# Optimization experiments

Hardware: AMD Instinct MI355X
Metric: run time of the kernel (lower is better)

Reference implementation:

```python
import jax, jax.numpy as jnp
import numpy as np

B, T, UD, YD, ZD, HD, L = 1024, 1024, 16, 16, 16, 128, 2


def setup_inputs() -> dict:
    key = jax.random.key(0)
    ks = iter(jax.random.split(key, 40))
    r = lambda *s: jax.random.normal(next(ks), s, jnp.float32) * 0.05
    inp = dict(
        u=jax.random.normal(next(ks), (B, UD, T), jnp.float32),
        y=jax.random.normal(next(ks), (B, YD, T), jnp.float32),
        h0=jax.random.uniform(next(ks), (L, B, HD), jnp.float32),
        phi_u_w0=r(HD, UD), phi_u_b0=r(HD), phi_u_w1=r(HD, HD), phi_u_b1=r(HD),
        dynn_w0=r(HD, 2 * HD), dynn_b0=r(HD), dynn_w1=r(HD, HD), dynn_b1=r(HD),
        x_mean_w=r(ZD, HD), x_mean_b=r(ZD),
        x_logvar_w=r(ZD, HD), x_logvar_b=r(ZD),
        phi_x_w0=r(HD, 2 * ZD), phi_x_b0=r(HD), phi_x_w1=r(HD, HD), phi_x_b1=r(HD),
        menn_w0=r(HD, HD), menn_b0=r(HD), menn_w1=r(YD, HD), menn_b1=r(YD),
        gru_wih=r(L, 3 * HD, HD), gru_whh=r(L, 3 * HD, HD),
        C=r(YD, ZD),
    )
    return inp


def _mlp2(x, w0, b0, w1, b1):
    # Linear -> ReLU -> Linear (torch Linear: y = x W^T + b)
    return jax.nn.relu(x @ w0.T + b0) @ w1.T + b1


def reference(u, y, h0,
              phi_u_w0, phi_u_b0, phi_u_w1, phi_u_b1,
              dynn_w0, dynn_b0, dynn_w1, dynn_b1,
              x_mean_w, x_mean_b, x_logvar_w, x_logvar_b,
              phi_x_w0, phi_x_b0, phi_x_w1, phi_x_b1,
              menn_w0, menn_b0, menn_w1, menn_b1,
              gru_wih, gru_whh, C):
    uT = jnp.moveaxis(u, 2, 0)  # (T, B, UD)
    yT = jnp.moveaxis(y, 2, 0)  # (T, B, YD)

    def step(h, xy):
        u_t, y_t = xy
        phi_u_t = _mlp2(u_t, phi_u_w0, phi_u_b0, phi_u_w1, phi_u_b1)  # (B, HD)
        dphi = _mlp2(jnp.concatenate([phi_u_t, h[-1]], axis=1),
                     dynn_w0, dynn_b0, dynn_w1, dynn_b1)
        x_mean = dphi @ x_mean_w.T + x_mean_b      # (B, ZD)
        x_logvar = dphi @ x_logvar_w.T + x_logvar_b
        # single-step multi-layer GRU (no bias), PyTorch gate order r,z,n
        x = phi_u_t
        hs = []
        for l in range(L):
            gi = x @ gru_wih[l].T          # (B, 3HD)
            gh = h[l] @ gru_whh[l].T
            ir, iz, inn = jnp.split(gi, 3, axis=1)
            hr, hz, hn = jnp.split(gh, 3, axis=1)
            rg = jax.nn.sigmoid(ir + hr)
            zg = jax.nn.sigmoid(iz + hz)
            ng = jnp.tanh(inn + rg * hn)
            hl = (1.0 - zg) * ng + zg * h[l]
            hs.append(hl)
            x = hl
        h_new = jnp.stack(hs, axis=0)
        # mpnt_wt >= 10 branch: NN measurement + physics measurement C @ x_mean
        phi_x = _mlp2(jnp.concatenate([x_mean, x_logvar], axis=1),
                      phi_x_w0, phi_x_b0, phi_x_w1, phi_x_b1)
        y_hat = _mlp2(phi_x, menn_w0, menn_b0, menn_w1, menn_b1) + x_mean @ C.T
        loss_t = jnp.sum((y_hat - y_t) ** 2)
        return h_new, loss_t

    _, losses = jax.lax.scan(step, h0, (uT, yT))
    return jnp.sum(losses)
```

## Files before the change

### kernel.cpp

```cpp
#include <hip/hip_runtime.h>
#include <hip/hip_bf16.h>

typedef unsigned short u16;
typedef unsigned int u32;
using short8 = __attribute__((ext_vector_type(8))) short;
using f32x4  = __attribute__((ext_vector_type(4))) float;

#define DEVINL static __device__ __forceinline__

DEVINL float bf2f(u16 u){
  union { unsigned int i; float f; } x; x.i = ((unsigned int)u) << 16; return x.f;
}
DEVINL u16 f2bf(float f){
  union { float f; unsigned int i; } x; x.f = f;
  unsigned int i = x.i;
  return (u16)((i + 0x7FFFu + ((i >> 16) & 1u)) >> 16);
}
DEVINL u16 f2bf1(float f){
  __hip_bfloat16 b = __float2bfloat16(f);
  u16 u; __builtin_memcpy(&u, &b, 2); return u;
}
DEVINL float fast_sigm(float x){
  float e = __builtin_amdgcn_exp2f(x * -1.442695041f);
  return __builtin_amdgcn_rcpf(1.f + e);
}
DEVINL float fast_tanh(float x){
  x = fminf(fmaxf(x, -10.f), 10.f);
  float e = __builtin_amdgcn_exp2f(x * -2.885390082f);
  return (1.f - e) * __builtin_amdgcn_rcpf(1.f + e);
}
DEVINL f32x4 zero4(){ f32x4 z = {0.f, 0.f, 0.f, 0.f}; return z; }

DEVINL f32x4 mfma16(short8 a, short8 b, f32x4 c){
  return __builtin_amdgcn_mfma_f32_16x16x32_bf16(a, b, c, 0, 0, 0);
}

DEVINL short8 frag_ld(const u16* base, int stride){
  int l = threadIdx.x & 63;
  return *(const short8*)(base + (l & 15) * stride + ((l >> 4) << 3));
}
DEVINL short8 gfrag(const u16* rowbase, int stride, int ks){
  int l = threadIdx.x & 63;
  return *(const short8*)(rowbase + (size_t)(l & 15) * stride + ks * 32 + ((l >> 4) << 3));
}

DEVINL void acc_store_lds(u16* dst, int stride, int col_base, f32x4 acc, float bias, bool relu){
  int l = threadIdx.x & 63;
  int col = col_base + (l & 15);
  int row0 = (l >> 4) * 4;
  #pragma unroll
  for (int r = 0; r < 4; r++){
    float v = acc[r] + bias;
    if (relu) v = fmaxf(v, 0.f);
    dst[(row0 + r) * stride + col] = f2bf(v);
  }
}

DEVINL void stage_weights(u16* dst, const float* src, int N, int K, int Kp){
  int stride = Kp + 8;
  if (Kp > K){
    int padw = Kp - K;
    for (int i = threadIdx.x; i < N * padw; i += blockDim.x){
      int n = i / padw, k = K + (i - (i / padw) * padw);
      dst[n * stride + k] = 0;
    }
  }
  for (int i = threadIdx.x * 4; i < N * K; i += blockDim.x * 4){
    float4 v = *(const float4*)(src + i);
    int n = i / K, k = i - n * K;
    u16* d = dst + n * stride + k;
    d[0] = f2bf(v.x); d[1] = f2bf(v.y); d[2] = f2bf(v.z); d[3] = f2bf(v.w);
  }
}

__global__ __launch_bounds__(256) void k_inith(const float* __restrict__ h0, u16* __restrict__ hst){
  int i = blockIdx.x * 256 + threadIdx.x;
  if (i < 2 * 1024 * 128) hst[i] = f2bf(h0[i]);
}

__global__ __launch_bounds__(512, 4) void k_phiu(const float* __restrict__ u,
    const float* __restrict__ w0, const float* __restrict__ b0,
    const float* __restrict__ w1, const float* __restrict__ b1,
    u16* __restrict__ phi, int t0, int Tc){
  __shared__ __align__(16) u16 w0s[128 * 40];
  __shared__ __align__(16) u16 w1s[128 * 136];
  __shared__ __align__(16) u16 buf[8][16 * 136];
  stage_weights(w0s, w0, 128, 16, 32);
  stage_weights(w1s, w1, 128, 128, 128);
  int wv = threadIdx.x >> 6, l = threadIdx.x & 63;
  u16* mybuf = buf[wv];
  float b0v[8], b1v[8];
  #pragma unroll
  for (int nt = 0; nt < 8; nt++){
    b0v[nt] = b0[nt * 16 + (l & 15)];
    b1v[nt] = b1[nt * 16 + (l & 15)];
  }
  __syncthreads();
  int tpb = Tc >> 4;
  int ntile = 1024 * tpb;
  int stride = gridDim.x * 8;
  for (int tile = blockIdx.x * 8 + wv; tile < ntile; tile += stride){
    int b = tile / tpb;
    int tt = (tile - b * tpb) << 4;
    int t = l & 15, kb = l >> 4;
    #pragma unroll
    for (int j = 0; j < 4; j++){
      int k = kb + j * 4;
      mybuf[t * 136 + k] = f2bf(u[(size_t)(b * 16 + k) * 1024 + t0 + tt + t]);
      mybuf[t * 136 + 16 + k] = 0;
    }
    short8 a0 = frag_ld(mybuf, 136);
    f32x4 acc[8];
    #pragma unroll
    for (int nt = 0; nt < 8; nt++)
      acc[nt] = mfma16(a0, frag_ld(w0s + nt * 16 * 40, 40), zero4());
    #pragma unroll
    for (int nt = 0; nt < 8; nt++)
      acc_store_lds(mybuf, 136, nt * 16, acc[nt], b0v[nt], true);
    f32x4 a2[8];
    #pragma unroll
    for (int nt = 0; nt < 8; nt++) a2[nt] = zero4();
    #pragma unroll
    for (int ks = 0; ks < 4; ks++){
      short8 a = frag_ld(mybuf + ks * 32, 136);
      #pragma unroll
      for (int nt = 0; nt < 8; nt++)
        a2[nt] = mfma16(a, frag_ld(w1s + nt * 16 * 136 + ks * 32, 136), a2[nt]);
    }
    #pragma unroll
    for (int nt = 0; nt < 8; nt++)
      acc_store_lds(mybuf, 136, nt * 16, a2[nt], b1v[nt], false);
    u16* dst = phi + (size_t)(b * Tc + tt) * 128;
    #pragma unroll
    for (int j = 0; j < 4; j++){
      int c = j * 64 + l;
      int row = c >> 4, k = (c & 15) * 8;
      *(short8*)(dst + row * 128 + k) = *(const short8*)(mybuf + row * 136 + k);
    }
  }
}

__global__ __launch_bounds__(256, 1) void k_gru(const u16* __restrict__ phi,
    const float* __restrict__ gwih, const float* __restrict__ gwhh,
    u16* __restrict__ hst, u16* __restrict__ Hs, int Tc){
  __shared__ __align__(16) u16 wi0[384 * 136];
  __shared__ __align__(16) u16 h0s[2][16 * 136];
  __shared__ __align__(16) u16 h1s[2][16 * 136];
  __shared__ __align__(16) u16 pb[4][16 * 136];
  const int l = threadIdx.x & 63;
  const int wv = threadIdx.x >> 6;
  const int b0 = blockIdx.x * 16;
  const int m0 = (l >> 4) * 4;
  const int cc = l & 15;
  const int nb = wv * 32;

  stage_weights(wi0, gwih, 384, 128, 128);

  const float* srcs[3] = { gwhh, gwih + 49152, gwhh + 49152 };
  short8 Wr[3][3][2][4];
  #pragma unroll
  for (int mm = 0; mm < 3; mm++){
    #pragma unroll
    for (int g = 0; g < 3; g++){
      #pragma unroll
      for (int nt = 0; nt < 2; nt++){
        int n = g * 128 + nb + nt * 16 + cc;
        #pragma unroll
        for (int ks = 0; ks < 4; ks++){
          const float* p = srcs[mm] + (size_t)n * 128 + ks * 32 + ((l >> 4) << 3);
          float4 va = *(const float4*)p;
          float4 vb = *(const float4*)(p + 4);
          short8 f;
          f[0] = (short)f2bf(va.x); f[1] = (short)f2bf(va.y);
          f[2] = (short)f2bf(va.z); f[3] = (short)f2bf(va.w);
          f[4] = (short)f2bf(vb.x); f[5] = (short)f2bf(vb.y);
          f[6] = (short)f2bf(vb.z); f[7] = (short)f2bf(vb.w);
          Wr[mm][g][nt][ks] = f;
        }
      }
    }
  }
  const int row = threadIdx.x >> 4, k0 = (threadIdx.x & 15) * 8;
  *(uint4*)(&h0s[0][row * 136 + k0]) = *(const uint4*)(hst + (size_t)(b0 + row) * 128 + k0);
  *(uint4*)(&h1s[0][row * 136 + k0]) = *(const uint4*)(hst + 131072 + (size_t)(b0 + row) * 128 + k0);
  float hp0[2][4], hp1[2][4];
  #pragma unroll
  for (int nt = 0; nt < 2; nt++)
    #pragma unroll
    for (int r = 0; r < 4; r++){
      hp0[nt][r] = bf2f(hst[(size_t)(b0 + m0 + r) * 128 + nb + nt * 16 + cc]);
      hp1[nt][r] = bf2f(hst[131072 + (size_t)(b0 + m0 + r) * 128 + nb + nt * 16 + cc]);
    }
  const u16* pL = phi + (size_t)(b0 + row) * Tc * 128 + k0;
  u16* Hp = Hs + (size_t)(b0 + row) * Tc * 128 + k0;
  *(uint4*)(&pb[0][row * 136 + k0]) = *(const uint4*)(pL);
  *(uint4*)(&pb[1][row * 136 + k0]) = *(const uint4*)(pL + 128);
  uint4 pfA = *(const uint4*)(pL + 2 * 128);
  uint4 pfB = *(const uint4*)(pL + 3 * 128);
  __syncthreads();

  auto ITER = [&](int i, int P, int q, uint4& pf){
    short8 a0[4];
    #pragma unroll
    for (int ks = 0; ks < 4; ks++) a0[ks] = frag_ld(h0s[P] + ks * 32, 136);
    if (i > 0){
      short8 a1[4];
      #pragma unroll
      for (int ks = 0; ks < 4; ks++) a1[ks] = frag_ld(h1s[P ^ 1] + ks * 32, 136);
      *(uint4*)(Hp + (size_t)(i - 1) * 128) = *(const uint4*)(&h1s[P ^ 1][row * 136 + k0]);
      f32x4 cr[2], cz[2], cin[2], chn[2];
      #pragma unroll
      for (int nt = 0; nt < 2; nt++){ cr[nt]=zero4(); cz[nt]=zero4(); cin[nt]=zero4(); chn[nt]=zero4(); }
      #pragma unroll
      for (int ks = 0; ks < 4; ks++)
        #pragma unroll
        for (int nt = 0; nt < 2; nt++){
          cr[nt]  = mfma16(a0[ks], Wr[1][0][nt][ks], cr[nt]);
          cr[nt]  = mfma16(a1[ks], Wr[2][0][nt][ks], cr[nt]);
          cz[nt]  = mfma16(a0[ks], Wr[1][1][nt][ks], cz[nt]);
          cz[nt]  = mfma16(a1[ks], Wr[2][1][nt][ks], cz[nt]);
          cin[nt] = mfma16(a0[ks], Wr[1][2][nt][ks], cin[nt]);
          chn[nt] = mfma16(a1[ks], Wr[2][2][nt][ks], chn[nt]);
        }
      #pragma unroll
      for (int nt = 0; nt < 2; nt++)
        #pragma unroll
        for (int r = 0; r < 4; r++){
          float rg = fast_sigm(cr[nt][r]);
          float zg = fast_sigm(cz[nt][r]);
          float ng = fast_tanh(cin[nt][r] + rg * chn[nt][r]);
          float hv = zg * (hp1[nt][r] - ng) + ng;
          hp1[nt][r] = hv;
          h1s[P][(m0 + r) * 136 + nb + nt * 16 + cc] = f2bf1(hv);
        }
    }
    if (i < Tc){
      short8 ap[4];
      #pragma unroll
      for (int ks = 0; ks < 4; ks++) ap[ks] = frag_ld(pb[q] + ks * 32, 136);
      f32x4 cr[2], cz[2], cin[2], chn[2];
      #pragma unroll
      for (int nt = 0; nt < 2; nt++){ cr[nt]=zero4(); cz[nt]=zero4(); cin[nt]=zero4(); chn[nt]=zero4(); }
      #pragma unroll
      for (int ks = 0; ks < 4; ks++)
        #pragma unroll
        for (int nt = 0; nt < 2; nt++){
          cr[nt]  = mfma16(ap[ks], frag_ld(wi0 + (0 * 128 + nb + nt * 16) * 136 + ks * 32, 136), cr[nt]);
          cr[nt]  = mfma16(a0[ks], Wr[0][0][nt][ks], cr[nt]);
          cz[nt]  = mfma16(ap[ks], frag_ld(wi0 + (1 * 128 + nb + nt * 16) * 136 + ks * 32, 136), cz[nt]);
          cz[nt]  = mfma16(a0[ks], Wr[0][1][nt][ks], cz[nt]);
          cin[nt] = mfma16(ap[ks], frag_ld(wi0 + (2 * 128 + nb + nt * 16) * 136 + ks * 32, 136), cin[nt]);
          chn[nt] = mfma16(a0[ks], Wr[0][2][nt][ks], chn[nt]);
        }
      if (i + 2 < Tc) *(uint4*)(&pb[(q + 2) & 3][row * 136 + k0]) = pf;
      if (i + 4 < Tc) pf = *(const uint4*)(pL + (size_t)(i + 4) * 128);
      #pragma unroll
      for (int nt = 0; nt < 2; nt++)
        #pragma unroll
        for (int r = 0; r < 4; r++){
          float rg = fast_sigm(cr[nt][r]);
          float zg = fast_sigm(cz[nt][r]);
          float ng = fast_tanh(cin[nt][r] + rg * chn[nt][r]);
          float hv = zg * (hp0[nt][r] - ng) + ng;
          hp0[nt][r] = hv;
          h0s[P ^ 1][(m0 + r) * 136 + nb + nt * 16 + cc] = f2bf1(hv);
        }
    }
    asm volatile("s_waitcnt lgkmcnt(0)" ::: "memory");
    __builtin_amdgcn_s_barrier();
    asm volatile("" ::: "memory");
  };

  for (int i = 0; i < Tc; i += 4){
    ITER(i + 0, 0, 0, pfA);
    ITER(i + 1, 1, 1, pfB);
    ITER(i + 2, 0, 2, pfA);
    ITER(i + 3, 1, 3, pfB);
  }
  ITER(Tc, 0, 0, pfA);
  *(uint4*)(hst + (size_t)(b0 + row) * 128 + k0) = *(const uint4*)(&h0s[0][row * 136 + k0]);
  *(uint4*)(hst + 131072 + (size_t)(b0 + row) * 128 + k0) = *(const uint4*)(&h1s[0][row * 136 + k0]);
}

__global__ __launch_bounds__(512, 2) void k_c1(const u16* __restrict__ phi, const u16* __restrict__ Hs,
    const float* __restrict__ dw0, const float* __restrict__ db0,
    const float* __restrict__ dw1, const float* __restrict__ db1,
    const float* __restrict__ xmw, const float* __restrict__ xmb,
    const float* __restrict__ xlw, const float* __restrict__ xlb,
    u16* __restrict__ xmlv, int Tc){
  __shared__ __align__(16) u16 w0s[128 * 264];
  __shared__ __align__(16) u16 w1s[128 * 136];
  __shared__ __align__(16) u16 xws[32 * 136];
  __shared__ __align__(16) u16 buf[8][16 * 136];
  stage_weights(w0s, dw0, 128, 256, 256);
  stage_weights(w1s, dw1, 128, 128, 128);
  stage_weights(xws, xmw, 16, 128, 128);
  stage_weights(xws + 16 * 136, xlw, 16, 128, 128);
  int wv = threadIdx.x >> 6, l = threadIdx.x & 63;
  u16* mybuf = buf[wv];
  float b0v[8], b1v[8];
  #pragma unroll
  for (int nt = 0; nt < 8; nt++){
    b0v[nt] = db0[nt * 16 + (l & 15)];
    b1v[nt] = db1[nt * 16 + (l & 15)];
  }
  float bxm = xmb[l & 15], bxl = xlb[l & 15];
  __syncthreads();
  int tpb = Tc >> 4;
  int ntile = 1024 * tpb;
  int stride = gridDim.x * 8;
  for (int tile = blockIdx.x * 8 + wv; tile < ntile; tile += stride){
    int b = tile / tpb;
    int tt = (tile - b * tpb) << 4;
    size_t rbase = (size_t)(b * Tc + tt);
    const u16* ap = phi + rbase * 128;
    const u16* hp = Hs + rbase * 128;
    f32x4 acc[8];
    #pragma unroll
    for (int nt = 0; nt < 8; nt++) acc[nt] = zero4();
    #pragma unroll
    for (int ks = 0; ks < 8; ks++){
      short8 a = (ks < 4) ? gfrag(ap, 128, ks) : gfrag(hp, 128, ks - 4);
      #pragma unroll
      for (int nt = 0; nt < 8; nt++)
        acc[nt] = mfma16(a, frag_ld(w0s + nt * 16 * 264 + ks * 32, 264), acc[nt]);
    }
    #pragma unroll
    for (int nt = 0; nt < 8; nt++)
      acc_store_lds(mybuf, 136, nt * 16, acc[nt], b0v[nt], true);
    f32x4 a2[8];
    #pragma unroll
    for (int nt = 0; nt < 8; nt++) a2[nt] = zero4();
    #pragma unroll
    for (int ks = 0; ks < 4; ks++){
      short8 a = frag_ld(mybuf + ks * 32, 136);
      #pragma unroll
      for (int nt = 0; nt < 8; nt++)
        a2[nt] = mfma16(a, frag_ld(w1s + nt * 16 * 136 + ks * 32, 136), a2[nt]);
    }
    #pragma unroll
    for (int nt = 0; nt < 8; nt++)
      acc_store_lds(mybuf, 136, nt * 16, a2[nt], b1v[nt], false);
    f32x4 am = zero4(), al = zero4();
    #pragma unroll
    for (int ks = 0; ks < 4; ks++){
      short8 a = frag_ld(mybuf + ks * 32, 136);
      am = mfma16(a, frag_ld(xws + ks * 32, 136), am);
      al = mfma16(a, frag_ld(xws + 16 * 136 + ks * 32, 136), al);
    }
    acc_store_lds(mybuf, 136, 0, am, bxm, false);
    acc_store_lds(mybuf, 136, 16, al, bxl, false);
    u16* dst = xmlv + rbase * 32;
    int c = l;
    int row = c >> 2, k = (c & 3) * 8;
    *(short8*)(dst + row * 32 + k) = *(const short8*)(mybuf + row * 136 + k);
  }
}

__global__ __launch_bounds__(512, 2) void k_c2(const u16* __restrict__ xmlv, const float* __restrict__ y,
    const float* __restrict__ pw0, const float* __restrict__ pb0,
    const float* __restrict__ pw1, const float* __restrict__ pb1,
    const float* __restrict__ mw0, const float* __restrict__ mb0,
    const float* __restrict__ mw1, const float* __restrict__ mb1,
    const float* __restrict__ Cw, float* __restrict__ out, int t0, int Tc){
  __shared__ __align__(16) u16 pw0s[128 * 40];
  __shared__ __align__(16) u16 pw1s[128 * 136];
  __shared__ __align__(16) u16 mw0s[128 * 136];
  __shared__ __align__(16) u16 mw1s[16 * 136];
  __shared__ __align__(16) u16 Cs[16 * 40];
  __shared__ __align__(16) u16 buf[8][16 * 136];
  stage_weights(pw0s, pw0, 128, 32, 32);
  stage_weights(pw1s, pw1, 128, 128, 128);
  stage_weights(mw0s, mw0, 128, 128, 128);
  stage_weights(mw1s, mw1, 16, 128, 128);
  stage_weights(Cs, Cw, 16, 16, 32);
  int wv = threadIdx.x >> 6, l = threadIdx.x & 63;
  u16* mybuf = buf[wv];
  float bp0v[8], bp1v[8], bm0v[8];
  #pragma unroll
  for (int nt = 0; nt < 8; nt++){
    bp0v[nt] = pb0[nt * 16 + (l & 15)];
    bp1v[nt] = pb1[nt * 16 + (l & 15)];
    bm0v[nt] = mb0[nt * 16 + (l & 15)];
  }
  float bm1 = mb1[l & 15];
  __syncthreads();
  float lacc = 0.f;
  int tpb = Tc >> 4;
  int ntile = 1024 * tpb;
  int stride = gridDim.x * 8;
  for (int tile = blockIdx.x * 8 + wv; tile < ntile; tile += stride){
    int b = tile / tpb;
    int tt = (tile - b * tpb) << 4;
    size_t rbase = (size_t)(b * Tc + tt);
    const u16* xp = xmlv + rbase * 32;
    short8 a0 = gfrag(xp, 32, 0);
    f32x4 acc[8];
    #pragma unroll
    for (int nt = 0; nt < 8; nt++)
      acc[nt] = mfma16(a0, frag_ld(pw0s + nt * 16 * 40, 40), zero4());
    #pragma unroll
    for (int nt = 0; nt < 8; nt++)
      acc_store_lds(mybuf, 136, nt * 16, acc[nt], bp0v[nt], true);
    f32x4 a2[8];
    #pragma unroll
    for (int nt = 0; nt < 8; nt++) a2[nt] = zero4();
    #pragma unroll
    for (int ks = 0; ks < 4; ks++){
      short8 a = frag_ld(mybuf + ks * 32, 136);
      #pragma unroll
      for (int nt = 0; nt < 8; nt++)
        a2[nt] = mfma16(a, frag_ld(pw1s + nt * 16 * 136 + ks * 32, 136), a2[nt]);
    }
    #pragma unroll
    for (int nt = 0; nt < 8; nt++)
      acc_store_lds(mybuf, 136, nt * 16, a2[nt], bp1v[nt], false);
    f32x4 a3[8];
    #pragma unroll
    for (int nt = 0; nt < 8; nt++) a3[nt] = zero4();
    #pragma unroll
    for (int ks = 0; ks < 4; ks++){
      short8 a = frag_ld(mybuf + ks * 32, 136);
      #pragma unroll
      for (int nt = 0; nt < 8; nt++)
        a3[nt] = mfma16(a, frag_ld(mw0s + nt * 16 * 136 + ks * 32, 136), a3[nt]);
    }
    #pragma unroll
    for (int nt = 0; nt < 8; nt++)
      acc_store_lds(mybuf, 136, nt * 16, a3[nt], bm0v[nt], true);
    f32x4 ay = zero4();
    #pragma unroll
    for (int ks = 0; ks < 4; ks++){
      short8 a = frag_ld(mybuf + ks * 32, 136);
      ay = mfma16(a, frag_ld(mw1s + ks * 32, 136), ay);
    }
    f32x4 ac = mfma16(a0, frag_ld(Cs, 40), zero4());
    #pragma unroll
    for (int r = 0; r < 4; r++){
      float yh = ay[r] + bm1 + ac[r];
      int m = (l >> 4) * 4 + r, j = l & 15;
      float d = yh - y[(size_t)(b * 16 + j) * 1024 + t0 + tt + m];
      lacc += d * d;
    }
  }
  #pragma unroll
  for (int off = 32; off > 0; off >>= 1)
    lacc += __shfl_down(lacc, off);
  if (l == 0) atomicAdd(out, lacc);
}

extern "C" void kernel_launch(void* const* d_in, const int* in_sizes, int n_in,
                              void* d_out, int out_size, void* d_ws, size_t ws_size,
                              hipStream_t stream){
  const float* u    = (const float*)d_in[0];
  const float* y    = (const float*)d_in[1];
  const float* h0   = (const float*)d_in[2];
  const float* puw0 = (const float*)d_in[3];
  const float* pub0 = (const float*)d_in[4];
  const float* puw1 = (const float*)d_in[5];
  const float* pub1 = (const float*)d_in[6];
  const float* dw0  = (const float*)d_in[7];
  const float* db0  = (const float*)d_in[8];
  const float* dw1  = (const float*)d_in[9];
  const float* db1  = (const float*)d_in[10];
  const float* xmw  = (const float*)d_in[11];
  const float* xmb  = (const float*)d_in[12];
  const float* xlw  = (const float*)d_in[13];
  const float* xlb  = (const float*)d_in[14];
  const float* pxw0 = (const float*)d_in[15];
  const float* pxb0 = (const float*)d_in[16];
  const float* pxw1 = (const float*)d_in[17];
  const float* pxb1 = (const float*)d_in[18];
  const float* mw0  = (const float*)d_in[19];
  const float* mb0  = (const float*)d_in[20];
  const float* mw1  = (const float*)d_in[21];
  const float* mb1  = (const float*)d_in[22];
  const float* gwih = (const float*)d_in[23];
  const float* gwhh = (const float*)d_in[24];
  const float* Cw   = (const float*)d_in[25];

  char* w = (char*)d_ws;
  u16* hst = (u16*)w; w += (size_t)2 * 1024 * 128 * 2;
  size_t head = (size_t)2 * 1024 * 128 * 2 + 4096;
  size_t avail = (ws_size > head) ? (ws_size - head) : 0;
  int Tc = 1024;
  while (Tc > 64 && (size_t)1024 * (size_t)Tc * (128 + 128 + 32) * 2 > avail) Tc >>= 1;
  u16* phi  = (u16*)w; w += (size_t)1024 * Tc * 128 * 2;
  u16* Hs   = (u16*)w; w += (size_t)1024 * Tc * 128 * 2;
  u16* xmlv = (u16*)w; w += (size_t)1024 * Tc * 32 * 2;

  hipMemsetAsync(d_out, 0, sizeof(float), stream);
  k_inith<<<1024, 256, 0, stream>>>(h0, hst);
  for (int t0 = 0; t0 < 1024; t0 += Tc){
    k_phiu<<<512, 512, 0, stream>>>(u, puw0, pub0, puw1, pub1, phi, t0, Tc);
    k_gru<<<64, 256, 0, stream>>>(phi, gwih, gwhh, hst, Hs, Tc);
    k_c1<<<256, 512, 0, stream>>>(phi, Hs, dw0, db0, dw1, db1, xmw, xmb, xlw, xlb, xmlv, Tc);
    k_c2<<<256, 512, 0, stream>>>(xmlv, y, pxw0, pxb0, pxw1, pxb1, mw0, mb0, mw1, mb1, Cw,
                                  (float*)d_out, t0, Tc);
  }
}
```

Before: 3.378 ms.

## Split GRU layers across two warp groups with register-resident weights

The GRU kernel now launches 512 threads per block instead of 256. The first four waves compute layer 0 and the other four compute layer 1 of the wavefront-pipelined recurrence. Each group holds its own input and hidden weights in registers, so the LDS-staged layer-0 input weights and their per-step LDS fragment loads are gone. s_setprio is raised around the MFMA chains. This should roughly halve the serial MFMA work per wave on the recurrent critical path, at the cost of more waves competing for the same CU and the barrier now spanning eight waves.

```diff
diff --git a/kernel.cpp b/kernel.cpp
--- a/kernel.cpp
+++ b/kernel.cpp
@@ -140,26 +140,24 @@
   }
 }
 
-__global__ __launch_bounds__(256, 1) void k_gru(const u16* __restrict__ phi,
+__global__ __launch_bounds__(512, 1) void k_gru(const u16* __restrict__ phi,
     const float* __restrict__ gwih, const float* __restrict__ gwhh,
     u16* __restrict__ hst, u16* __restrict__ Hs, int Tc){
-  __shared__ __align__(16) u16 wi0[384 * 136];
   __shared__ __align__(16) u16 h0s[2][16 * 136];
   __shared__ __align__(16) u16 h1s[2][16 * 136];
   __shared__ __align__(16) u16 pb[4][16 * 136];
   const int l = threadIdx.x & 63;
-  const int wv = threadIdx.x >> 6;
+  const bool isL0 = (threadIdx.x < 256);
+  const int wv4 = (threadIdx.x >> 6) & 3;
   const int b0 = blockIdx.x * 16;
   const int m0 = (l >> 4) * 4;
   const int cc = l & 15;
-  const int nb = wv * 32;
-
-  stage_weights(wi0, gwih, 384, 128, 128);
-
-  const float* srcs[3] = { gwhh, gwih + 49152, gwhh + 49152 };
-  short8 Wr[3][3][2][4];
-  #pragma unroll
-  for (int mm = 0; mm < 3; mm++){
+  const int nb = wv4 * 32;
+
+  const float* wsrc[2] = { isL0 ? gwih : gwih + 49152, isL0 ? gwhh : gwhh + 49152 };
+  short8 Wr[2][3][2][4];
+  #pragma unroll
+  for (int mm = 0; mm < 2; mm++){
     #pragma unroll
     for (int g = 0; g < 3; g++){
       #pragma unroll
@@ -167,7 +165,7 @@
         int n = g * 128 + nb + nt * 16 + cc;
         #pragma unroll
         for (int ks = 0; ks < 4; ks++){
-          const float* p = srcs[mm] + (size_t)n * 128 + ks * 32 + ((l >> 4) << 3);
+          const float* p = wsrc[mm] + (size_t)n * 128 + ks * 32 + ((l >> 4) << 3);
           float4 va = *(const float4*)p;
           float4 vb = *(const float4*)(p + 4);
           short8 f;
@@ -180,91 +178,108 @@
       }
     }
   }
-  const int row = threadIdx.x >> 4, k0 = (threadIdx.x & 15) * 8;
-  *(uint4*)(&h0s[0][row * 136 + k0]) = *(const uint4*)(hst + (size_t)(b0 + row) * 128 + k0);
-  *(uint4*)(&h1s[0][row * 136 + k0]) = *(const uint4*)(hst + 131072 + (size_t)(b0 + row) * 128 + k0);
-  float hp0[2][4], hp1[2][4];
+  {
+    int row = threadIdx.x >> 5, k0 = (threadIdx.x & 31) * 4;
+    *(uint2*)(&h0s[0][row * 136 + k0]) = *(const uint2*)(hst + (size_t)(b0 + row) * 128 + k0);
+    *(uint2*)(&h1s[0][row * 136 + k0]) = *(const uint2*)(hst + 131072 + (size_t)(b0 + row) * 128 + k0);
+  }
+  const u16* hbase = hst + (isL0 ? 0 : 131072);
+  float hp[2][4];
   #pragma unroll
   for (int nt = 0; nt < 2; nt++)
     #pragma unroll
-    for (int r = 0; r < 4; r++){
-      hp0[nt][r] = bf2f(hst[(size_t)(b0 + m0 + r) * 128 + nb + nt * 16 + cc]);
-      hp1[nt][r] = bf2f(hst[131072 + (size_t)(b0 + m0 + r) * 128 + nb + nt * 16 + cc]);
-    }
-  const u16* pL = phi + (size_t)(b0 + row) * Tc * 128 + k0;
-  u16* Hp = Hs + (size_t)(b0 + row) * Tc * 128 + k0;
-  *(uint4*)(&pb[0][row * 136 + k0]) = *(const uint4*)(pL);
-  *(uint4*)(&pb[1][row * 136 + k0]) = *(const uint4*)(pL + 128);
-  uint4 pfA = *(const uint4*)(pL + 2 * 128);
-  uint4 pfB = *(const uint4*)(pL + 3 * 128);
+    for (int r = 0; r < 4; r++)
+      hp[nt][r] = bf2f(hbase[(size_t)(b0 + m0 + r) * 128 + nb + nt * 16 + cc]);
+
+  const int gp = threadIdx.x & 255;
+  const int srow = gp >> 4, sk = (gp & 15) * 8;
+  const u16* pL0 = phi + (size_t)(b0 + srow) * Tc * 128 + sk;
+  u16* Hp = Hs + (size_t)(b0 + srow) * Tc * 128 + sk;
+  uint4 pfA, pfB;
+  if (isL0){
+    *(uint4*)(&pb[0][srow * 136 + sk]) = *(const uint4*)(pL0);
+    *(uint4*)(&pb[1][srow * 136 + sk]) = *(const uint4*)(pL0 + 128);
+    pfA = *(const uint4*)(pL0 + 2 * 128);
+    pfB = *(const uint4*)(pL0 + 3 * 128);
+  }
   __syncthreads();
 
   auto ITER = [&](int i, int P, int q, uint4& pf){
-    short8 a0[4];
-    #pragma unroll
-    for (int ks = 0; ks < 4; ks++) a0[ks] = frag_ld(h0s[P] + ks * 32, 136);
-    if (i > 0){
-      short8 a1[4];
-      #pragma unroll
-      for (int ks = 0; ks < 4; ks++) a1[ks] = frag_ld(h1s[P ^ 1] + ks * 32, 136);
-      *(uint4*)(Hp + (size_t)(i - 1) * 128) = *(const uint4*)(&h1s[P ^ 1][row * 136 + k0]);
-      f32x4 cr[2], cz[2], cin[2], chn[2];
-      #pragma unroll
-      for (int nt = 0; nt < 2; nt++){ cr[nt]=zero4(); cz[nt]=zero4(); cin[nt]=zero4(); chn[nt]=zero4(); }
-      #pragma unroll
-      for (int ks = 0; ks < 4; ks++)
-        #pragma unroll
-        for (int nt = 0; nt < 2; nt++){
-          cr[nt]  = mfma16(a0[ks], Wr[1][0][nt][ks], cr[nt]);
-          cr[nt]  = mfma16(a1[ks], Wr[2][0][nt][ks], cr[nt]);
-          cz[nt]  = mfma16(a0[ks], Wr[1][1][nt][ks], cz[nt]);
-          cz[nt]  = mfma16(a1[ks], Wr[2][1][nt][ks], cz[nt]);
-          cin[nt] = mfma16(a0[ks], Wr[1][2][nt][ks], cin[nt]);
-          chn[nt] = mfma16(a1[ks], Wr[2][2][nt][ks], chn[nt]);
+    if (isL0){
+      if (i < Tc){
+        short8 a0[4], ap[4];
+        #pragma unroll
+        for (int ks = 0; ks < 4; ks++){
+          a0[ks] = frag_ld(h0s[P] + ks * 32, 136);
+          ap[ks] = frag_ld(pb[q] + ks * 32, 136);
         }
-      #pragma unroll
-      for (int nt = 0; nt < 2; nt++)
-        #pragma unroll
-        for (int r = 0; r < 4; r++){
-          float rg = fast_sigm(cr[nt][r]);
-          float zg = fast_sigm(cz[nt][r]);
-          float ng = fast_tanh(cin[nt][r] + rg * chn[nt][r]);
-          float hv = zg * (hp1[nt][r] - ng) + ng;
-          hp1[nt][r] = hv;
-          h1s[P][(m0 + r) * 136 + nb + nt * 16 + cc] = f2bf1(hv);
+        f32x4 cr[2], cz[2], cin[2], chn[2];
+        #pragma unroll
+        for (int nt = 0; nt < 2; nt++){ cr[nt]=zero4(); cz[nt]=zero4(); cin[nt]=zero4(); chn[nt]=zero4(); }
+        __builtin_amdgcn_s_setprio(1);
+        #pragma unroll
+        for (int ks = 0; ks < 4; ks++)
+          #pragma unroll
+          for (int nt = 0; nt < 2; nt++){
+            cr[nt]  = mfma16(ap[ks], Wr[0][0][nt][ks], cr[nt]);
+            cr[nt]  = mfma16(a0[ks], Wr[1][0][nt][ks], cr[nt]);
+            cz[nt]  = mfma16(ap[ks], Wr[0][1][nt][ks], cz[nt]);
+            cz[nt]  = mfma16(a0[ks], Wr[1][1][nt][ks], cz[nt]);
+            cin[nt] = mfma16(ap[ks], Wr[0][2][nt][ks], cin[nt]);
+            chn[nt] = mfma16(a0[ks], Wr[1][2][nt][ks], chn[nt]);
+          }
+        __builtin_amdgcn_s_setprio(0);
+        if (i + 2 < Tc) *(uint4*)(&pb[(q + 2) & 3][srow * 136 + sk]) = pf;
+        if (i + 4 < Tc) pf = *(const uint4*)(pL0 + (size_t)(i + 4) * 128);
+        #pragma unroll
+        for (int nt = 0; nt < 2; nt++)
+          #pragma unroll
+          for (int r = 0; r < 4; r++){
+            float rg = fast_sigm(cr[nt][r]);
+            float zg = fast_sigm(cz[nt][r]);
+            float ng = fast_tanh(cin[nt][r] + rg * chn[nt][r]);
+            float hv = zg * (hp[nt][r] - ng) + ng;
+            hp[nt][r] = hv;
+            h0s[P ^ 1][(m0 + r) * 136 + nb + nt * 16 + cc] = f2bf1(hv);
+          }
+      }
+    } else {
+      if (i > 0){
+        short8 a0[4], a1[4];
+        #pragma unroll
+        for (int ks = 0; ks < 4; ks++){
+          a0[ks] = frag_ld(h0s[P] + ks * 32, 136);
+          a1[ks] = frag_ld(h1s[P ^ 1] + ks * 32, 136);
         }
-    }
-    if (i < Tc){
-      short8 ap[4];
-      #pragma unroll
-      for (int ks = 0; ks < 4; ks++) ap[ks] = frag_ld(pb[q] + ks * 32, 136);
-      f32x4 cr[2], cz[2], cin[2], chn[2];
-      #pragma unroll
-      for (int nt = 0; nt < 2; nt++){ cr[nt]=zero4(); cz[nt]=zero4(); cin[nt]=zero4(); chn[nt]=zero4(); }
-      #pragma unroll
-      for (int ks = 0; ks < 4; ks++)
-        #pragma unroll
-        for (int nt = 0; nt < 2; nt++){
-          cr[nt]  = mfma16(ap[ks], frag_ld(wi0 + (0 * 128 + nb + nt * 16) * 136 + ks * 32, 136), cr[nt]);
-          cr[nt]  = mfma16(a0[ks], Wr[0][0][nt][ks], cr[nt]);
-          cz[nt]  = mfma16(ap[ks], frag_ld(wi0 + (1 * 128 + nb + nt * 16) * 136 + ks * 32, 136), cz[nt]);
-          cz[nt]  = mfma16(a0[ks], Wr[0][1][nt][ks], cz[nt]);
-          cin[nt] = mfma16(ap[ks], frag_ld(wi0 + (2 * 128 + nb + nt * 16) * 136 + ks * 32, 136), cin[nt]);
-          chn[nt] = mfma16(a0[ks], Wr[0][2][nt][ks], chn[nt]);
-        }
-      if (i + 2 < Tc) *(uint4*)(&pb[(q + 2) & 3][row * 136 + k0]) = pf;
-      if (i + 4 < Tc) pf = *(const uint4*)(pL + (size_t)(i + 4) * 128);
-      #pragma unroll
-      for (int nt = 0; nt < 2; nt++)
-        #pragma unroll
-        for (int r = 0; r < 4; r++){
-          float rg = fast_sigm(cr[nt][r]);
-          float zg = fast_sigm(cz[nt][r]);
-          float ng = fast_tanh(cin[nt][r] + rg * chn[nt][r]);
-          float hv = zg * (hp0[nt][r] - ng) + ng;
-          hp0[nt][r] = hv;
-          h0s[P ^ 1][(m0 + r) * 136 + nb + nt * 16 + cc] = f2bf1(hv);
-        }
+        *(uint4*)(Hp + (size_t)(i - 1) * 128) = *(const uint4*)(&h1s[P ^ 1][srow * 136 + sk]);
+        f32x4 cr[2], cz[2], cin[2], chn[2];
+        #pragma unroll
+        for (int nt = 0; nt < 2; nt++){ cr[nt]=zero4(); cz[nt]=zero4(); cin[nt]=zero4(); chn[nt]=zero4(); }
+        __builtin_amdgcn_s_setprio(1);
+        #pragma unroll
+        for (int ks = 0; ks < 4; ks++)
+          #pragma unroll
+          for (int nt = 0; nt < 2; nt++){
+            cr[nt]  = mfma16(a0[ks], Wr[0][0][nt][ks], cr[nt]);
+            cr[nt]  = mfma16(a1[ks], Wr[1][0][nt][ks], cr[nt]);
+            cz[nt]  = mfma16(a0[ks], Wr[0][1][nt][ks], cz[nt]);
+            cz[nt]  = mfma16(a1[ks], Wr[1][1][nt][ks], cz[nt]);
+            cin[nt] = mfma16(a0[ks], Wr[0][2][nt][ks], cin[nt]);
+            chn[nt] = mfma16(a1[ks], Wr[1][2][nt][ks], chn[nt]);
+          }
+        __builtin_amdgcn_s_setprio(0);
+        #pragma unroll
+        for (int nt = 0; nt < 2; nt++)
+          #pragma unroll
+          for (int r = 0; r < 4; r++){
+            float rg = fast_sigm(cr[nt][r]);
+            float zg = fast_sigm(cz[nt][r]);
+            float ng = fast_tanh(cin[nt][r] + rg * chn[nt][r]);
+            float hv = zg * (hp[nt][r] - ng) + ng;
+            hp[nt][r] = hv;
+            h1s[P][(m0 + r) * 136 + nb + nt * 16 + cc] = f2bf1(hv);
+          }
+      }
     }
     asm volatile("s_waitcnt lgkmcnt(0)" ::: "memory");
     __builtin_amdgcn_s_barrier();
@@ -278,8 +293,11 @@
     ITER(i + 3, 1, 3, pfB);
   }
   ITER(Tc, 0, 0, pfA);
-  *(uint4*)(hst + (size_t)(b0 + row) * 128 + k0) = *(const uint4*)(&h0s[0][row * 136 + k0]);
-  *(uint4*)(hst + 131072 + (size_t)(b0 + row) * 128 + k0) = *(const uint4*)(&h1s[0][row * 136 + k0]);
+  {
+    int row = threadIdx.x >> 5, k0 = (threadIdx.x & 31) * 4;
+    *(uint2*)(hst + (size_t)(b0 + row) * 128 + k0) = *(const uint2*)(&h0s[0][row * 136 + k0]);
+    *(uint2*)(hst + 131072 + (size_t)(b0 + row) * 128 + k0) = *(const uint2*)(&h1s[0][row * 136 + k0]);
+  }
 }
 
 __global__ __launch_bounds__(512, 2) void k_c1(const u16* __restrict__ phi, const u16* __restrict__ Hs,
@@ -493,7 +511,7 @@
   k_inith<<<1024, 256, 0, stream>>>(h0, hst);
   for (int t0 = 0; t0 < 1024; t0 += Tc){
     k_phiu<<<512, 512, 0, stream>>>(u, puw0, pub0, puw1, pub1, phi, t0, Tc);
-    k_gru<<<64, 256, 0, stream>>>(phi, gwih, gwhh, hst, Hs, Tc);
+    k_gru<<<64, 512, 0, stream>>>(phi, gwih, gwhh, hst, Hs, Tc);
     k_c1<<<256, 512, 0, stream>>>(phi, Hs, dw0, db0, dw1, db1, xmw, xmb, xlw, xlb, xmlv, Tc);
     k_c2<<<256, 512, 0, stream>>>(xmlv, y, pxw0, pxb0, pxw1, pxb1, mw0, mb0, mw1, mb1, Cw,
                                   (float*)d_out, t0, Tc);
```

Result: slower. 3.737 ms (+10.6%).
